# Optimization experiments

Measured on AMD Instinct MI355X. Metric: run time of the kernel, lower is better.

The kernel has to match this reference:

```python
import jax, jax.numpy as jnp
import numpy as np

PADDING = 1
STRIDE = 1

def setup_inputs() -> dict:
    key = jax.random.key(0)
    k1, k2 = jax.random.split(key)
    x = jax.random.normal(k1, (32, 64, 64, 64), dtype=jnp.float32)
    # kaiming_normal fan_out, relu: std = sqrt(2 / (out_ch * k * k))
    fan_out = 128 * 3 * 3
    std = np.sqrt(2.0 / fan_out).astype(np.float32)
    weight = jax.random.normal(k2, (128, 64, 3, 3), dtype=jnp.float32) * std
    bias = jnp.zeros((128,), dtype=jnp.float32)
    return {"x": x, "weight": weight, "bias": bias}

def reference(x, weight, bias):
    # Faithful to the unfold+multiply+sum path, which computes a standard
    # cross-correlation conv2d (torch conv semantics) with stride/padding.
    out = jax.lax.conv_general_dilated(
        x, weight,
        window_strides=(STRIDE, STRIDE),
        padding=[(PADDING, PADDING), (PADDING, PADDING)],
        dimension_numbers=("NCHW", "OIHW", "NCHW"),
    )
    return out + bias[None, :, None, None]
```

## Files before the change

kernel.cpp:

```cpp
#include <hip/hip_runtime.h>


typedef short short8 __attribute__((ext_vector_type(8)));
typedef float f32x4  __attribute__((ext_vector_type(4)));

static __device__ __forceinline__ unsigned short f2bf(float f) {
    unsigned int u = __float_as_uint(f);
    u = (u + 0x7FFFu + ((u >> 16) & 1u)) >> 16;
    return (unsigned short)u;
}
static __device__ __forceinline__ unsigned int pk2(float lo, float hi) {
    return (unsigned int)f2bf(lo) | ((unsigned int)f2bf(hi) << 16);
}
static __device__ __forceinline__ void gload16(const void* g, void* l) {
    __builtin_amdgcn_global_load_lds(
        (const __attribute__((address_space(1))) void*)g,
        (__attribute__((address_space(3))) void*)l, 16, 0, 0);
}

__global__ __launch_bounds__(256)
void prep_xp(const float* __restrict__ x, unsigned short* __restrict__ xP)
{
    const int hp = blockIdx.x, n = blockIdx.y, tid = threadIdx.x;
    unsigned short* rowBase = xP + (((size_t)n * 66 + hp) * 66) * 64;
    if (hp == 0 || hp == 65) {
        uint4 z; z.x = z.y = z.z = z.w = 0u;
        for (int i = tid; i < 528; i += 256) ((uint4*)rowBase)[i] = z;
        return;
    }
    __shared__ float T[64][65];
    const int h = hp - 1;
    const size_t nbase = (size_t)n * 262144 + (size_t)h * 64;
    #pragma unroll
    for (int i = 0; i < 16; ++i) {
        int idx = tid + i * 256;
        int ci = idx >> 6, w = idx & 63;
        T[ci][w] = x[nbase + (size_t)ci * 4096 + w];
    }
    __syncthreads();
    if (tid < 16) {
        uint4 z; z.x = z.y = z.z = z.w = 0u;
        int wp = (tid >> 3) * 65;
        ((uint4*)(rowBase + wp * 64))[tid & 7] = z;
    }
    const int w = tid >> 2, cg = tid & 3;
    const int wp = w + 1;
    #pragma unroll
    for (int t = 0; t < 2; ++t) {
        const int g = cg * 2 + t;
        uint4 v;
        v.x = pk2(T[g*8+0][w], T[g*8+1][w]);
        v.y = pk2(T[g*8+2][w], T[g*8+3][w]);
        v.z = pk2(T[g*8+4][w], T[g*8+5][w]);
        v.w = pk2(T[g*8+6][w], T[g*8+7][w]);
        *(uint4*)(rowBase + wp * 64 + ((g ^ (wp & 7)) * 8)) = v;
    }
}

__global__ __launch_bounds__(256)
void prep_wS2(const float* __restrict__ w, unsigned short* __restrict__ wS)
{
    int u = blockIdx.x * 256 + threadIdx.x;
    if (u >= 9216) return;
    int slot = u & 3, co = (u >> 2) & 127, s = u >> 9;
    int p = s >> 1, ch = s & 1;
    int g = slot ^ (co & 3);
    const float* src = w + (size_t)(co * 64 + ch * 32 + g * 8) * 9 + p;
    uint4 v;
    v.x = pk2(src[0*9], src[1*9]);
    v.y = pk2(src[2*9], src[3*9]);
    v.z = pk2(src[4*9], src[5*9]);
    v.w = pk2(src[6*9], src[7*9]);
    *(uint4*)(wS + (size_t)u * 8) = v;
}

#define XWIN  50688
#define WHALF 8192
#define TOTAL_LDS (XWIN + 2*WHALF)

__global__ __launch_bounds__(512, 4)
void conv_mfma11(const unsigned short* __restrict__ xP,
                 const unsigned short* __restrict__ wS,
                 const float* __restrict__ bias,
                 float* __restrict__ out)
{
    extern __shared__ __align__(16) char lds[];
    char* wb = lds + XWIN;

    const int tid  = threadIdx.x;
    const int hq   = blockIdx.x;
    const int n    = blockIdx.y;
    const int h0   = hq * 4;
    const int wid  = tid >> 6, lane = tid & 63;
    const int cb   = wid >> 2;
    const int wrow = wid & 3;
    const int l15  = lane & 15, l4 = lane >> 4;

    const unsigned short* xPn = xP + (size_t)n * (66 * 66 * 64);
    const char* wSb = (const char*)wS;

    #pragma unroll
    for (int rr = 0; rr < 6; ++rr)
        gload16(xPn + (size_t)(h0 + rr) * 4224 + tid * 8, lds + rr * 8448 + tid * 16);
    if (lane < 16 && wid < 6)
        gload16(xPn + (size_t)(h0 + wid) * 4224 + (512 + lane) * 8, lds + wid * 8448 + 8192);
    gload16(wSb + tid * 16, wb + tid * 16);
    __syncthreads();

    f32x4 acc[4][4];
    #pragma unroll
    for (int mf = 0; mf < 4; ++mf)
        #pragma unroll
        for (int nf = 0; nf < 4; ++nf)
            acc[mf][nf] = (f32x4)0.0f;

    #pragma unroll
    for (int s = 0; s < 18; ++s) {
        const int p  = s >> 1;
        const int ch = s & 1;
        const int kh = p / 3, kw = p - kh * 3;

        if (s < 17)
            gload16(wSb + ((s + 1) * 512 + tid) * 16, wb + ((s + 1) & 1) * WHALF + tid * 16);

        const char* wcur = wb + (s & 1) * WHALF;
        const char* xrow = lds + (wrow + kh) * 8448;

        short8 Bf[4];
        #pragma unroll
        for (int nf = 0; nf < 4; ++nf) {
            const int wp = nf * 16 + l15 + kw;
            Bf[nf] = *(const short8*)(xrow + wp * 128 + (((ch * 4 + l4) ^ (wp & 7)) * 16));
        }
        #pragma unroll
        for (int mf = 0; mf < 4; ++mf) {
            const int co = cb * 64 + mf * 16 + l15;
            short8 Af = *(const short8*)(wcur + co * 64 + ((l4 ^ (co & 3)) * 16));
            #pragma unroll
            for (int nf = 0; nf < 4; ++nf)
                acc[mf][nf] = __builtin_amdgcn_mfma_f32_16x16x32_bf16(
                    Af, Bf[nf], acc[mf][nf], 0, 0, 0);
        }
        if (s < 17) __syncthreads();
    }

    {
        const int h = h0 + wrow;
        #pragma unroll
        for (int mf = 0; mf < 4; ++mf) {
            const f32x4 bv4 = *(const f32x4*)(bias + cb * 64 + mf * 16 + l4 * 4);
            #pragma unroll
            for (int r = 0; r < 4; ++r) {
                const int co = cb * 64 + mf * 16 + l4 * 4 + r;
                float* orow = out + (((size_t)n * 128 + co) * 64 + h) * 64;
                #pragma unroll
                for (int nf = 0; nf < 4; ++nf)
                    orow[nf * 16 + l15] = acc[mf][nf][r] + bv4[r];
            }
        }
    }
}

__global__ __launch_bounds__(256, 4)
void conv2d_f32_tiled(const float* __restrict__ x,
                      const float* __restrict__ wgt,
                      const float* __restrict__ bias,
                      float* __restrict__ out)
{
    __shared__ float Xlds[8][10][66];
    __shared__ float Wlds[32][72];
    const int tid = threadIdx.x;
    const int co0 = blockIdx.x * 32, h0 = blockIdx.y * 8, n = blockIdx.z;
    const int tco = tid >> 6, lane = tid & 63;
    float acc[8][8];
    #pragma unroll
    for (int i = 0; i < 8; ++i)
        #pragma unroll
        for (int j = 0; j < 8; ++j) acc[i][j] = 0.0f;
    for (int cc = 0; cc < 8; ++cc) {
        const int ci0 = cc * 8;
        for (int idx = tid; idx < 8 * 10 * 66; idx += 256) {
            const int ww = idx % 66, t = idx / 66, hh = t % 10, ci = t / 10;
            const int gh = h0 + hh - 1, gw = ww - 1;
            float v = 0.0f;
            if ((unsigned)gh < 64u && (unsigned)gw < 64u)
                v = x[(((size_t)n * 64 + ci0 + ci) * 64 + gh) * 64 + gw];
            Xlds[ci][hh][ww] = v;
        }
        for (int idx = tid; idx < 32 * 72; idx += 256) {
            const int r = idx % 72, co = idx / 72;
            Wlds[co][r] = wgt[(size_t)(co0 + co) * 576 + ci0 * 9 + r];
        }
        __syncthreads();
        for (int ci = 0; ci < 8; ++ci)
            #pragma unroll
            for (int kh = 0; kh < 3; ++kh)
                #pragma unroll
                for (int kw = 0; kw < 3; ++kw) {
                    float wv[8];
                    #pragma unroll
                    for (int i = 0; i < 8; ++i) wv[i] = Wlds[tco * 8 + i][ci * 9 + kh * 3 + kw];
                    #pragma unroll
                    for (int j = 0; j < 8; ++j) {
                        const float xv = Xlds[ci][j + kh][lane + kw];
                        #pragma unroll
                        for (int i = 0; i < 8; ++i) acc[i][j] = fmaf(wv[i], xv, acc[i][j]);
                    }
                }
        __syncthreads();
    }
    #pragma unroll
    for (int i = 0; i < 8; ++i) {
        const int co = co0 + tco * 8 + i;
        const float b = bias[co];
        #pragma unroll
        for (int j = 0; j < 8; ++j)
            out[(((size_t)n * 128 + co) * 64 + (h0 + j)) * 64 + lane] = acc[i][j] + b;
    }
}

extern "C" void kernel_launch(void* const* d_in, const int* in_sizes, int n_in,
                              void* d_out, int out_size, void* d_ws, size_t ws_size,
                              hipStream_t stream)
{
    const float* x    = (const float*)d_in[0];
    const float* wgt  = (const float*)d_in[1];
    const float* bias = (const float*)d_in[2];
    float* out        = (float*)d_out;

    const size_t XP_BYTES = (size_t)32 * 66 * 66 * 64 * 2;
    const size_t WS_BYTES = (size_t)9216 * 16;

    if (ws_size < XP_BYTES + WS_BYTES) {
        dim3 grid(4, 8, 32);
        conv2d_f32_tiled<<<grid, 256, 0, stream>>>(x, wgt, bias, out);
        return;
    }

    unsigned short* xP = (unsigned short*)d_ws;
    unsigned short* wS = (unsigned short*)((char*)d_ws + XP_BYTES);

    (void)hipFuncSetAttribute((const void*)conv_mfma11,
                              hipFuncAttributeMaxDynamicSharedMemorySize, TOTAL_LDS);

    prep_xp<<<dim3(66, 32), 256, 0, stream>>>(x, xP);
    prep_wS2<<<dim3(36), 256, 0, stream>>>(wgt, wS);
    conv_mfma11<<<dim3(16, 32), 512, TOTAL_LDS, stream>>>(xP, wS, bias, out);
}
```

Before: 45.95 us.

## Fuse input padding and bf16 conversion into conv kernel

Removes the separate prep_xp kernel that wrote a padded, swizzled bf16 copy of the input to workspace. The conv kernel now reads fp32 input directly, applies the zero padding, packs channel pairs to bf16 and writes them into the same swizzled LDS layout. This drops one launch and a full round trip of the converted tensor through global memory. In exchange the per-block loads become scalar, strided fp32 reads with bounds checks instead of async direct-to-LDS copies, and each block re-reads halo rows.

Result: slower. 53.18 us (+15.7%).

```diff
diff --git a/kernel.cpp b/kernel.cpp
--- a/kernel.cpp
+++ b/kernel.cpp
@@ -16,45 +16,6 @@
     __builtin_amdgcn_global_load_lds(
         (const __attribute__((address_space(1))) void*)g,
         (__attribute__((address_space(3))) void*)l, 16, 0, 0);
-}
-
-__global__ __launch_bounds__(256)
-void prep_xp(const float* __restrict__ x, unsigned short* __restrict__ xP)
-{
-    const int hp = blockIdx.x, n = blockIdx.y, tid = threadIdx.x;
-    unsigned short* rowBase = xP + (((size_t)n * 66 + hp) * 66) * 64;
-    if (hp == 0 || hp == 65) {
-        uint4 z; z.x = z.y = z.z = z.w = 0u;
-        for (int i = tid; i < 528; i += 256) ((uint4*)rowBase)[i] = z;
-        return;
-    }
-    __shared__ float T[64][65];
-    const int h = hp - 1;
-    const size_t nbase = (size_t)n * 262144 + (size_t)h * 64;
-    #pragma unroll
-    for (int i = 0; i < 16; ++i) {
-        int idx = tid + i * 256;
-        int ci = idx >> 6, w = idx & 63;
-        T[ci][w] = x[nbase + (size_t)ci * 4096 + w];
-    }
-    __syncthreads();
-    if (tid < 16) {
-        uint4 z; z.x = z.y = z.z = z.w = 0u;
-        int wp = (tid >> 3) * 65;
-        ((uint4*)(rowBase + wp * 64))[tid & 7] = z;
-    }
-    const int w = tid >> 2, cg = tid & 3;
-    const int wp = w + 1;
-    #pragma unroll
-    for (int t = 0; t < 2; ++t) {
-        const int g = cg * 2 + t;
-        uint4 v;
-        v.x = pk2(T[g*8+0][w], T[g*8+1][w]);
-        v.y = pk2(T[g*8+2][w], T[g*8+3][w]);
-        v.z = pk2(T[g*8+4][w], T[g*8+5][w]);
-        v.w = pk2(T[g*8+6][w], T[g*8+7][w]);
-        *(uint4*)(rowBase + wp * 64 + ((g ^ (wp & 7)) * 8)) = v;
-    }
 }
 
 __global__ __launch_bounds__(256)
@@ -79,10 +40,10 @@
 #define TOTAL_LDS (XWIN + 2*WHALF)
 
 __global__ __launch_bounds__(512, 4)
-void conv_mfma11(const unsigned short* __restrict__ xP,
-                 const unsigned short* __restrict__ wS,
-                 const float* __restrict__ bias,
-                 float* __restrict__ out)
+void conv_fused(const float* __restrict__ x,
+                const unsigned short* __restrict__ wS,
+                const float* __restrict__ bias,
+                float* __restrict__ out)
 {
     extern __shared__ __align__(16) char lds[];
     char* wb = lds + XWIN;
@@ -96,15 +57,27 @@
     const int wrow = wid & 3;
     const int l15  = lane & 15, l4 = lane >> 4;
 
-    const unsigned short* xPn = xP + (size_t)n * (66 * 66 * 64);
+    const float* xn = x + (size_t)n * 262144;
     const char* wSb = (const char*)wS;
 
-    #pragma unroll
-    for (int rr = 0; rr < 6; ++rr)
-        gload16(xPn + (size_t)(h0 + rr) * 4224 + tid * 8, lds + rr * 8448 + tid * 16);
-    if (lane < 16 && wid < 6)
-        gload16(xPn + (size_t)(h0 + wid) * 4224 + (512 + lane) * 8, lds + wid * 8448 + 8192);
     gload16(wSb + tid * 16, wb + tid * 16);
+
+    for (int idx = tid; idx < 12672; idx += 512) {
+        const int r   = idx / 2112;
+        const int rem = idx - r * 2112;
+        const int wp  = rem >> 5;
+        const int cp  = rem & 31;
+        const int gh  = h0 + r - 1;
+        const int gw  = wp - 1;
+        float a = 0.0f, b = 0.0f;
+        if ((unsigned)gh < 64u && (unsigned)gw < 64u) {
+            const float* s = xn + ((size_t)(cp * 2) * 64 + gh) * 64 + gw;
+            a = s[0];
+            b = s[4096];
+        }
+        *(unsigned int*)(lds + r * 8448 + wp * 128 +
+                         (((cp >> 2) ^ (wp & 7)) << 4) + ((cp & 3) << 2)) = pk2(a, b);
+    }
     __syncthreads();
 
     f32x4 acc[4][4];
@@ -228,22 +201,19 @@
     const float* bias = (const float*)d_in[2];
     float* out        = (float*)d_out;
 
-    const size_t XP_BYTES = (size_t)32 * 66 * 66 * 64 * 2;
     const size_t WS_BYTES = (size_t)9216 * 16;
 
-    if (ws_size < XP_BYTES + WS_BYTES) {
+    if (ws_size < WS_BYTES) {
         dim3 grid(4, 8, 32);
         conv2d_f32_tiled<<<grid, 256, 0, stream>>>(x, wgt, bias, out);
         return;
     }
 
-    unsigned short* xP = (unsigned short*)d_ws;
-    unsigned short* wS = (unsigned short*)((char*)d_ws + XP_BYTES);
-
-    (void)hipFuncSetAttribute((const void*)conv_mfma11,
+    unsigned short* wS = (unsigned short*)d_ws;
+
+    (void)hipFuncSetAttribute((const void*)conv_fused,
                               hipFuncAttributeMaxDynamicSharedMemorySize, TOTAL_LDS);
 
-    prep_xp<<<dim3(66, 32), 256, 0, stream>>>(x, xP);
     prep_wS2<<<dim3(36), 256, 0, stream>>>(wgt, wS);
-    conv_mfma11<<<dim3(16, 32), 512, TOTAL_LDS, stream>>>(xP, wS, bias, out);
-}
+    conv_fused<<<dim3(16, 32), 512, TOTAL_LDS, stream>>>(x, wS, bias, out);
+}
```

## Restructure conv to one output row per block with direct-from-global MFMA weight fragments

Applied to the files above, without the earlier changes.

Replaces the 4-row, 512-thread conv kernel with a 1-row, 256-thread kernel (2048 blocks) that stages only 3 input rows in LDS. Weights are pre-arranged into per-lane MFMA A-fragment order and read straight from global/L2 instead of being double-buffered through LDS with per-step barriers, which removes the 17 syncthreads in the main loop. It also adds s_setprio around the MFMA groups. The trade-off is that the same input rows are loaded by three times as many blocks (more redundant traffic) and weight fragments are fetched from cache by every block, with smaller per-wave tiles giving less reuse per load.

After: 53.50 us. 16.4% more time.

```diff
diff --git a/kernel.cpp b/kernel.cpp
--- a/kernel.cpp
+++ b/kernel.cpp
@@ -58,94 +58,87 @@
 }
 
 __global__ __launch_bounds__(256)
-void prep_wS2(const float* __restrict__ w, unsigned short* __restrict__ wS)
-{
-    int u = blockIdx.x * 256 + threadIdx.x;
-    if (u >= 9216) return;
-    int slot = u & 3, co = (u >> 2) & 127, s = u >> 9;
-    int p = s >> 1, ch = s & 1;
-    int g = slot ^ (co & 3);
-    const float* src = w + (size_t)(co * 64 + ch * 32 + g * 8) * 9 + p;
-    uint4 v;
-    v.x = pk2(src[0*9], src[1*9]);
-    v.y = pk2(src[2*9], src[3*9]);
-    v.z = pk2(src[4*9], src[5*9]);
-    v.w = pk2(src[6*9], src[7*9]);
-    *(uint4*)(wS + (size_t)u * 8) = v;
-}
-
-#define XWIN  50688
-#define WHALF 8192
-#define TOTAL_LDS (XWIN + 2*WHALF)
-
-__global__ __launch_bounds__(512, 4)
-void conv_mfma11(const unsigned short* __restrict__ xP,
-                 const unsigned short* __restrict__ wS,
+void prep_wA(const float* __restrict__ w, unsigned short* __restrict__ wA)
+{
+    int t = blockIdx.x * 256 + threadIdx.x;
+    if (t >= 73728) return;
+    int j    = t & 7;
+    int lane = (t >> 3) & 63;
+    int mf   = (t >> 9) & 3;
+    int c    = (t >> 11) & 1;
+    int rest = t >> 12;
+    int p    = rest % 9;
+    int cb   = rest / 9;
+    int co = cb * 64 + mf * 16 + (lane & 15);
+    int ci = c * 32 + (lane >> 4) * 8 + j;
+    wA[t] = f2bf(w[(size_t)(co * 64 + ci) * 9 + p]);
+}
+
+__global__ __launch_bounds__(256, 4)
+void conv_mfma13(const unsigned short* __restrict__ xP,
+                 const unsigned short* __restrict__ wA,
                  const float* __restrict__ bias,
                  float* __restrict__ out)
 {
-    extern __shared__ __align__(16) char lds[];
-    char* wb = lds + XWIN;
+    __shared__ __align__(16) char lds[25344];
 
     const int tid  = threadIdx.x;
-    const int hq   = blockIdx.x;
+    const int h    = blockIdx.x;
     const int n    = blockIdx.y;
-    const int h0   = hq * 4;
     const int wid  = tid >> 6, lane = tid & 63;
-    const int cb   = wid >> 2;
-    const int wrow = wid & 3;
+    const int cb   = wid >> 1;
+    const int sh   = wid & 1;
     const int l15  = lane & 15, l4 = lane >> 4;
 
     const unsigned short* xPn = xP + (size_t)n * (66 * 66 * 64);
-    const char* wSb = (const char*)wS;
-
-    #pragma unroll
-    for (int rr = 0; rr < 6; ++rr)
-        gload16(xPn + (size_t)(h0 + rr) * 4224 + tid * 8, lds + rr * 8448 + tid * 16);
-    if (lane < 16 && wid < 6)
-        gload16(xPn + (size_t)(h0 + wid) * 4224 + (512 + lane) * 8, lds + wid * 8448 + 8192);
-    gload16(wSb + tid * 16, wb + tid * 16);
+    const unsigned short* wAb = wA + (size_t)cb * 36864;
+
+    #pragma unroll
+    for (int k = 0; k < 7; ++k) {
+        int G = tid + k * 256;
+        if (k < 6 || tid < 48) {
+            int r = G / 528, gr = G - r * 528;
+            gload16(xPn + ((size_t)(h + r) * 528 + gr) * 8, lds + r * 8448 + gr * 16);
+        }
+    }
     __syncthreads();
 
-    f32x4 acc[4][4];
-    #pragma unroll
-    for (int mf = 0; mf < 4; ++mf)
-        #pragma unroll
-        for (int nf = 0; nf < 4; ++nf)
-            acc[mf][nf] = (f32x4)0.0f;
-
-    #pragma unroll
-    for (int s = 0; s < 18; ++s) {
-        const int p  = s >> 1;
-        const int ch = s & 1;
+    f32x4 acc[2][4];
+    f32x4 a00=(f32x4)0.f,a01=(f32x4)0.f,a10=(f32x4)0.f,a11=(f32x4)0.f;
+    f32x4 a20=(f32x4)0.f,a21=(f32x4)0.f,a30=(f32x4)0.f,a31=(f32x4)0.f;
+    (void)acc;
+
+    #pragma unroll
+    for (int p = 0; p < 9; ++p) {
         const int kh = p / 3, kw = p - kh * 3;
-
-        if (s < 17)
-            gload16(wSb + ((s + 1) * 512 + tid) * 16, wb + ((s + 1) & 1) * WHALF + tid * 16);
-
-        const char* wcur = wb + (s & 1) * WHALF;
-        const char* xrow = lds + (wrow + kh) * 8448;
-
-        short8 Bf[4];
-        #pragma unroll
-        for (int nf = 0; nf < 4; ++nf) {
-            const int wp = nf * 16 + l15 + kw;
-            Bf[nf] = *(const short8*)(xrow + wp * 128 + (((ch * 4 + l4) ^ (wp & 7)) * 16));
-        }
-        #pragma unroll
-        for (int mf = 0; mf < 4; ++mf) {
-            const int co = cb * 64 + mf * 16 + l15;
-            short8 Af = *(const short8*)(wcur + co * 64 + ((l4 ^ (co & 3)) * 16));
+        const char* xrow = lds + kh * 8448;
+        #pragma unroll
+        for (int c = 0; c < 2; ++c) {
+            short8 Bf[2];
             #pragma unroll
-            for (int nf = 0; nf < 4; ++nf)
-                acc[mf][nf] = __builtin_amdgcn_mfma_f32_16x16x32_bf16(
-                    Af, Bf[nf], acc[mf][nf], 0, 0, 0);
-        }
-        if (s < 17) __syncthreads();
+            for (int nf = 0; nf < 2; ++nf) {
+                const int wp = sh * 32 + nf * 16 + l15 + kw;
+                Bf[nf] = *(const short8*)(xrow + wp * 128 + (((c * 4 + l4) ^ (wp & 7)) * 16));
+            }
+            short8 Af0 = *(const short8*)(wAb + ((((p * 2 + c) * 4 + 0) * 64 + lane) << 3));
+            short8 Af1 = *(const short8*)(wAb + ((((p * 2 + c) * 4 + 1) * 64 + lane) << 3));
+            short8 Af2 = *(const short8*)(wAb + ((((p * 2 + c) * 4 + 2) * 64 + lane) << 3));
+            short8 Af3 = *(const short8*)(wAb + ((((p * 2 + c) * 4 + 3) * 64 + lane) << 3));
+            __builtin_amdgcn_s_setprio(1);
+            a00 = __builtin_amdgcn_mfma_f32_16x16x32_bf16(Af0, Bf[0], a00, 0, 0, 0);
+            a01 = __builtin_amdgcn_mfma_f32_16x16x32_bf16(Af0, Bf[1], a01, 0, 0, 0);
+            a10 = __builtin_amdgcn_mfma_f32_16x16x32_bf16(Af1, Bf[0], a10, 0, 0, 0);
+            a11 = __builtin_amdgcn_mfma_f32_16x16x32_bf16(Af1, Bf[1], a11, 0, 0, 0);
+            a20 = __builtin_amdgcn_mfma_f32_16x16x32_bf16(Af2, Bf[0], a20, 0, 0, 0);
+            a21 = __builtin_amdgcn_mfma_f32_16x16x32_bf16(Af2, Bf[1], a21, 0, 0, 0);
+            a30 = __builtin_amdgcn_mfma_f32_16x16x32_bf16(Af3, Bf[0], a30, 0, 0, 0);
+            a31 = __builtin_amdgcn_mfma_f32_16x16x32_bf16(Af3, Bf[1], a31, 0, 0, 0);
+            __builtin_amdgcn_s_setprio(0);
+        }
     }
 
     {
-        const int h = h0 + wrow;
+        f32x4 am[4][2] = {{a00,a01},{a10,a11},{a20,a21},{a30,a31}};
         #pragma unroll
         for (int mf = 0; mf < 4; ++mf) {
             const f32x4 bv4 = *(const f32x4*)(bias + cb * 64 + mf * 16 + l4 * 4);
@@ -154,8 +147,8 @@
                 const int co = cb * 64 + mf * 16 + l4 * 4 + r;
                 float* orow = out + (((size_t)n * 128 + co) * 64 + h) * 64;
                 #pragma unroll
-                for (int nf = 0; nf < 4; ++nf)
-                    orow[nf * 16 + l15] = acc[mf][nf][r] + bv4[r];
+                for (int nf = 0; nf < 2; ++nf)
+                    orow[sh * 32 + nf * 16 + l15] = am[mf][nf][r] + bv4[r];
             }
         }
     }
@@ -229,21 +222,18 @@
     float* out        = (float*)d_out;
 
     const size_t XP_BYTES = (size_t)32 * 66 * 66 * 64 * 2;
-    const size_t WS_BYTES = (size_t)9216 * 16;
-
-    if (ws_size < XP_BYTES + WS_BYTES) {
+    const size_t WA_BYTES = (size_t)73728 * 2;
+
+    if (ws_size < XP_BYTES + WA_BYTES) {
         dim3 grid(4, 8, 32);
         conv2d_f32_tiled<<<grid, 256, 0, stream>>>(x, wgt, bias, out);
         return;
     }
 
     unsigned short* xP = (unsigned short*)d_ws;
-    unsigned short* wS = (unsigned short*)((char*)d_ws + XP_BYTES);
-
-    (void)hipFuncSetAttribute((const void*)conv_mfma11,
-                              hipFuncAttributeMaxDynamicSharedMemorySize, TOTAL_LDS);
+    unsigned short* wA = (unsigned short*)((char*)d_ws + XP_BYTES);
 
     prep_xp<<<dim3(66, 32), 256, 0, stream>>>(x, xP);
-    prep_wS2<<<dim3(36), 256, 0, stream>>>(wgt, wS);
-    conv_mfma11<<<dim3(16, 32), 512, TOTAL_LDS, stream>>>(xP, wS, bias, out);
-}
+    prep_wA<<<dim3((73728 + 255) / 256), 256, 0, stream>>>(wgt, wA);
+    conv_mfma13<<<dim3(64, 32), 256, 0, stream>>>(xP, wA, bias, out);
+}
```
